# Performance work log

Hardware: AMD Instinct MI355X
Metric: run time of the kernel (lower is better)

The kernel has to match this reference:

```python
import jax, jax.numpy as jnp
import numpy as np

SEQ_LEN = 8192
VOCAB = 128000
EMB = 10   # embedding_size hard-coded in RNNLM.__init__
HID = 10   # hidden_size hard-coded


def setup_inputs() -> dict:
    key = jax.random.key(0)
    k1, k2, k3, k4, k5, k6 = jax.random.split(key, 6)
    input_batch = jax.random.randint(k1, (SEQ_LEN, 1), 0, VOCAB, dtype=jnp.int32)
    embedding = jax.random.normal(k2, (VOCAB, EMB), dtype=jnp.float32)
    # nn.Linear(input+hidden -> hidden) and nn.Linear(input+hidden -> vocab)
    W_i2h = jax.random.normal(k3, (HID, EMB + HID), dtype=jnp.float32) * 0.1
    b_i2h = jax.random.normal(k4, (HID,), dtype=jnp.float32) * 0.1
    W_i2o = jax.random.normal(k5, (VOCAB, EMB + HID), dtype=jnp.float32) * 0.1
    b_i2o = jax.random.normal(k6, (VOCAB,), dtype=jnp.float32) * 0.1
    return {
        "input_batch": input_batch,
        "embedding": embedding,
        "W_i2h": W_i2h,
        "b_i2h": b_i2h,
        "W_i2o": W_i2o,
        "b_i2o": b_i2o,
    }


def reference(input_batch, embedding, W_i2h, b_i2h, W_i2o, b_i2o):
    # Elman RNN unrolled over time via lax.scan; batch is 1 (required by the
    # original torch.cat of [B,10] embedding with [1,10] hidden state).
    def step(hidden, word_ix):
        w = embedding[word_ix]                              # (1, EMB)
        combined = jnp.concatenate([w, hidden], axis=1)     # (1, EMB+HID)
        new_hidden = combined @ W_i2h.T + b_i2h             # (1, HID)
        logits = combined @ W_i2o.T + b_i2o                 # (1, VOCAB)
        logp = jax.nn.log_softmax(logits, axis=1)
        pred = jnp.argmax(logp, axis=1).astype(jnp.float32)  # topk(1) index
        return new_hidden, pred

    hidden0 = jnp.zeros((1, HID), dtype=jnp.float32)
    _, preds = jax.lax.scan(step, hidden0, input_batch)     # preds: (SEQ_LEN, 1)
    return preds
```

## Files before the change

### kernel.cpp

```cpp
#include <hip/hip_runtime.h>

#define SEQ   8192
#define VOCAB 128000
#define L     64
#define NCH   128

#define OFF_CMB    0
#define OFF_CVEC   163840
#define OFF_AMAX   245760
#define OFF_AMAX1  262144
#define OFF_CNORM  270336
#define OFF_WPART  278528
#define OFF_WMAX   279040
#define OFF_C32    279104
#define OFF_W32    410176

#define CSL    160
#define CVSPAN 800
#define CNIT   25
#define SSL    64
#define SVSPAN 512
#define SNIT   16
#define CCAP   2048

typedef __attribute__((ext_vector_type(8))) short bf16x8;
typedef __attribute__((ext_vector_type(4))) float f32x4;

static __device__ inline unsigned short f2bf(float x) {
    unsigned u = __float_as_uint(x);
    u += 0x7FFF + ((u >> 16) & 1);
    return (unsigned short)(u >> 16);
}
static __device__ inline unsigned sortable(float x) {
    unsigned u = __float_as_uint(x);
    return (u & 0x80000000u) ? ~u : (u | 0x80000000u);
}
static __device__ inline float unsortable(unsigned k) {
    unsigned u = (k & 0x80000000u) ? (k & 0x7FFFFFFFu) : ~k;
    return __uint_as_float(u);
}

__global__ void k_prep(const int* __restrict__ ix, const float* __restrict__ emb,
                       const float* __restrict__ Wih, const float* __restrict__ bih,
                       const float* __restrict__ Wio, const float* __restrict__ bio,
                       float* __restrict__ ws) {
    int b = blockIdx.x;
    int tid = threadIdx.x;
    if (b < 32) {
        int t = b * 256 + tid;
        ((unsigned long long*)(ws + OFF_AMAX))[t] = 0ULL;
        ((unsigned*)(ws + OFF_AMAX1))[t] = 0u;

        int id = ix[t];
        float w[10];
        const float2* ep = (const float2*)(emb + (long long)id * 10);
#pragma unroll
        for (int j = 0; j < 5; j++) ((float2*)w)[j] = ep[j];
#pragma unroll
        for (int j = 0; j < 10; j++) ws[OFF_CMB + j * SEQ + t] = w[j];

        int m = t >> 6, k = t & 63;
        float* cv = ws + OFF_CVEC + (k * NCH + m) * 10;
#pragma unroll
        for (int i = 0; i < 10; i++) {
            float s = bih[i];
#pragma unroll
            for (int j = 0; j < 10; j++) s += Wih[i * 20 + j] * w[j];
            cv[i] = s;
        }
    } else {
        __shared__ float red[4];
        int bs = b - 32;
        int v = bs * 256 + tid;
        float w[20];
        const float4* r = (const float4*)(Wio + (long long)v * 20);
#pragma unroll
        for (int q = 0; q < 5; q++) ((float4*)w)[q] = r[q];
        float bv = bio[v];
        float n2 = bv * bv;
#pragma unroll
        for (int k = 0; k < 20; k++) n2 += w[k] * w[k];
        float nrm = sqrtf(n2);
        for (int off = 1; off < 64; off <<= 1)
            nrm = fmaxf(nrm, __shfl_xor(nrm, off));
        if ((tid & 63) == 0) red[tid >> 6] = nrm;
        __syncthreads();
        if (tid == 0)
            ws[OFF_WPART + bs] = fmaxf(fmaxf(red[0], red[1]), fmaxf(red[2], red[3]));

        unsigned short h[32];
#pragma unroll
        for (int k = 0; k < 20; k++) h[k] = f2bf(w[k]);
        h[20] = f2bf(bv);
#pragma unroll
        for (int k = 21; k < 32; k++) h[k] = 0;
        uint4* dst = (uint4*)((unsigned short*)(ws + OFF_W32));
#pragma unroll
        for (int i = 0; i < 4; i++) {
            uint4 u;
            u.x = (unsigned)h[8*i+0] | ((unsigned)h[8*i+1] << 16);
            u.y = (unsigned)h[8*i+2] | ((unsigned)h[8*i+3] << 16);
            u.z = (unsigned)h[8*i+4] | ((unsigned)h[8*i+5] << 16);
            u.w = (unsigned)h[8*i+6] | ((unsigned)h[8*i+7] << 16);
            dst[v * 4 + i] = u;
        }
    }
}

__global__ void k_scan(const float* __restrict__ Wih, float* __restrict__ ws) {
    __shared__ float P[100], Q[100];
    __shared__ float Dl[NCH][10];
    __shared__ float Hst[NCH][10];
    __shared__ float Hl[10];
    int tid = threadIdx.x;

    float Ar[10][10];
#pragma unroll
    for (int i = 0; i < 10; i++)
#pragma unroll
        for (int j = 0; j < 10; j++) Ar[i][j] = Wih[i * 20 + 10 + j];

    {
        int m = tid;
        float h[10];
#pragma unroll
        for (int i = 0; i < 10; i++) h[i] = 0.f;
        const float* cvb = ws + OFF_CVEC;
        float2 buf[5];
        {
            const float2* cp = (const float2*)(cvb + m * 10);
#pragma unroll
            for (int j = 0; j < 5; j++) buf[j] = cp[j];
        }
        for (int k = 0; k < L; k++) {
            float cc[10];
#pragma unroll
            for (int j = 0; j < 5; j++) { cc[2*j] = buf[j].x; cc[2*j+1] = buf[j].y; }
            if (k + 1 < L) {
                const float2* cp = (const float2*)(cvb + ((k + 1) * NCH + m) * 10);
#pragma unroll
                for (int j = 0; j < 5; j++) buf[j] = cp[j];
            }
            float nh[10];
#pragma unroll
            for (int i = 0; i < 10; i++) {
                float s = cc[i];
#pragma unroll
                for (int j = 0; j < 10; j++) s += Ar[i][j] * h[j];
                nh[i] = s;
            }
#pragma unroll
            for (int i = 0; i < 10; i++) h[i] = nh[i];
        }
#pragma unroll
        for (int i = 0; i < 10; i++) Dl[m][i] = h[i];
    }

    if (tid < 100) P[tid] = Wih[(tid / 10) * 20 + 10 + (tid % 10)];
    __syncthreads();
    for (int it = 0; it < 6; it++) {
        if (tid < 100) {
            int i = tid / 10, j = tid % 10;
            float s = 0.f;
#pragma unroll
            for (int k = 0; k < 10; k++) s += P[i * 10 + k] * P[k * 10 + j];
            Q[tid] = s;
        }
        __syncthreads();
        if (tid < 100) P[tid] = Q[tid];
        __syncthreads();
    }

    if (tid < 10) Hl[tid] = 0.f;
    __syncthreads();
    if (tid < 10) {
        int i = tid;
        float a64[10];
#pragma unroll
        for (int j = 0; j < 10; j++) a64[j] = P[i * 10 + j];
        float hc = 0.f;
        for (int m = 0; m < NCH; m++) {
            Hst[m][i] = hc;
            float s = Dl[m][i];
#pragma unroll
            for (int j = 0; j < 10; j++) s += a64[j] * Hl[j];
            Hl[i] = s;
            hc = s;
        }
    }
    __syncthreads();

    {
        int m = tid;
        float h[10];
#pragma unroll
        for (int i = 0; i < 10; i++) h[i] = Hst[m][i];
        const float* cvb = ws + OFF_CVEC;
        float2 buf[5];
        {
            const float2* cp = (const float2*)(cvb + m * 10);
#pragma unroll
            for (int j = 0; j < 5; j++) buf[j] = cp[j];
        }
        for (int k = 0; k < L; k++) {
            int tg = m * 64 + k;
            float cc[10];
#pragma unroll
            for (int j = 0; j < 5; j++) { cc[2*j] = buf[j].x; cc[2*j+1] = buf[j].y; }
            if (k + 1 < L) {
                const float2* cp = (const float2*)(cvb + ((k + 1) * NCH + m) * 10);
#pragma unroll
                for (int j = 0; j < 5; j++) buf[j] = cp[j];
            }
#pragma unroll
            for (int i = 0; i < 10; i++) ws[OFF_CMB + (10 + i) * SEQ + tg] = h[i];
            float nh[10];
#pragma unroll
            for (int i = 0; i < 10; i++) {
                float s = cc[i];
#pragma unroll
                for (int j = 0; j < 10; j++) s += Ar[i][j] * h[j];
                nh[i] = s;
            }
#pragma unroll
            for (int i = 0; i < 10; i++) h[i] = nh[i];
        }
    }
}

__global__ void k_pack_c(float* __restrict__ ws) {
    int b = blockIdx.x;
    int tid = threadIdx.x;
    if (b == 32) {
        __shared__ float red[4];
        float m = 0.f;
        for (int i = tid; i < 500; i += 256) m = fmaxf(m, ws[OFF_WPART + i]);
        for (int off = 1; off < 64; off <<= 1)
            m = fmaxf(m, __shfl_xor(m, off));
        if ((tid & 63) == 0) red[tid >> 6] = m;
        __syncthreads();
        if (tid == 0)
            ws[OFF_WMAX] = fmaxf(fmaxf(red[0], red[1]), fmaxf(red[2], red[3]));
        return;
    }
    int t = b * 256 + tid;
    float c[20];
#pragma unroll
    for (int k = 0; k < 20; k++) c[k] = ws[OFF_CMB + k * SEQ + t];
    float n2 = 1.0f;
#pragma unroll
    for (int k = 0; k < 20; k++) n2 += c[k] * c[k];
    ws[OFF_CNORM + t] = sqrtf(n2);

    unsigned short h[32];
#pragma unroll
    for (int k = 0; k < 20; k++) h[k] = f2bf(c[k]);
    h[20] = f2bf(1.0f);
#pragma unroll
    for (int k = 21; k < 32; k++) h[k] = 0;
    uint4* dst = (uint4*)((unsigned short*)(ws + OFF_C32));
#pragma unroll
    for (int i = 0; i < 4; i++) {
        uint4 u;
        u.x = (unsigned)h[8*i+0] | ((unsigned)h[8*i+1] << 16);
        u.y = (unsigned)h[8*i+2] | ((unsigned)h[8*i+3] << 16);
        u.z = (unsigned)h[8*i+4] | ((unsigned)h[8*i+5] << 16);
        u.w = (unsigned)h[8*i+6] | ((unsigned)h[8*i+7] << 16);
        dst[t * 4 + i] = u;
    }
}

__global__ __launch_bounds__(256, 4)
void k_seed(const float* __restrict__ ws, unsigned* __restrict__ amax1) {
    int tid = threadIdx.x;
    int lane = tid & 63, wid = tid >> 6, quad = lane >> 4, col = lane & 15;
    int r  = blockIdx.x & 7;
    int u  = blockIdx.x >> 3;
    int sl = r * 8 + (u & 7);
    int tb = u >> 3;
    int t0w = tb * 512 + wid * 128;
    int v0s = sl * SVSPAN;

    const unsigned short* c32 = (const unsigned short*)(ws + OFF_C32);
    const unsigned short* Wg  = (const unsigned short*)(ws + OFF_W32);

    bf16x8 a[8];
#pragma unroll
    for (int tt = 0; tt < 8; tt++)
        a[tt] = *(const bf16x8*)(c32 + (t0w + tt * 16 + col) * 32 + quad * 8);

    const f32x4 zero = {0.f, 0.f, 0.f, 0.f};
    float run[8][4];
#pragma unroll
    for (int tt = 0; tt < 8; tt++)
#pragma unroll
        for (int g = 0; g < 4; g++) run[tt][g] = -3.4e38f;

    const unsigned short* Wb = Wg + (unsigned)(v0s + col) * 32 + quad * 8;
    bf16x8 nb0 = *(const bf16x8*)(Wb);
    bf16x8 nb1 = *(const bf16x8*)(Wb + 512);

    for (int p = 0; p < SNIT; ++p) {
        bf16x8 b0 = nb0, b1 = nb1;
        int pn = (p + 1 < SNIT) ? p + 1 : p;
        const unsigned short* Wn = Wb + pn * 1024;
        nb0 = *(const bf16x8*)(Wn);
        nb1 = *(const bf16x8*)(Wn + 512);
#pragma unroll
        for (int tt = 0; tt < 8; tt++) {
            f32x4 d0 = __builtin_amdgcn_mfma_f32_16x16x32_bf16(a[tt], b0, zero, 0, 0, 0);
            f32x4 d1 = __builtin_amdgcn_mfma_f32_16x16x32_bf16(a[tt], b1, zero, 0, 0, 0);
#pragma unroll
            for (int g = 0; g < 4; g++)
                run[tt][g] = fmaxf(run[tt][g], fmaxf(d0[g], d1[g]));
        }
    }

#pragma unroll
    for (int tt = 0; tt < 8; tt++)
#pragma unroll
        for (int g = 0; g < 4; g++) {
            float r2 = run[tt][g];
            for (int off = 1; off < 16; off <<= 1)
                r2 = fmaxf(r2, __shfl_xor(r2, off));
            if (col == 0)
                atomicMax(&amax1[t0w + tt * 16 + quad * 4 + g], sortable(r2));
        }
}

__global__ __launch_bounds__(256, 4)
void k_cand(const float* __restrict__ ws, const float* __restrict__ Wio,
            const float* __restrict__ bio, const unsigned* __restrict__ amax1,
            unsigned long long* __restrict__ amax) {
    __shared__ unsigned cand[CCAP];
    __shared__ unsigned cnt;

    int tid = threadIdx.x;
    int lane = tid & 63, wid = tid >> 6, quad = lane >> 4, col = lane & 15;
    int r  = blockIdx.x & 7;
    int u  = blockIdx.x >> 3;
    int sl = r * 20 + (u % 20);
    int tb = u / 20;
    int t0w = tb * 512 + wid * 128;
    int v0s = sl * CVSPAN;
    if (tid == 0) cnt = 0;
    __syncthreads();

    const unsigned short* c32 = (const unsigned short*)(ws + OFF_C32);
    const unsigned short* Wg  = (const unsigned short*)(ws + OFF_W32);
    float wmax = ws[OFF_WMAX];

    bf16x8 a[8];
    f32x4 thrC[8];
#pragma unroll
    for (int tt = 0; tt < 8; tt++) {
        a[tt] = *(const bf16x8*)(c32 + (t0w + tt * 16 + col) * 32 + quad * 8);
#pragma unroll
        for (int g = 0; g < 4; g++) {
            int t = t0w + tt * 16 + quad * 4 + g;
            thrC[tt][g] = (0.04f * ws[OFF_CNORM + t] * wmax + 1e-5f)
                          - unsortable(amax1[t]);
        }
    }

    const unsigned short* Wb = Wg + (unsigned)(v0s + col) * 32 + quad * 8;
    bf16x8 nb0 = *(const bf16x8*)(Wb);
    bf16x8 nb1 = *(const bf16x8*)(Wb + 512);

    unsigned mask[8];
#pragma unroll
    for (int tt = 0; tt < 8; tt++) mask[tt] = 0u;

    for (int p = 0; p < CNIT; ++p) {
        bf16x8 b0 = nb0, b1 = nb1;
        int pn = (p + 1 < CNIT) ? p + 1 : p;
        const unsigned short* Wn = Wb + pn * 1024;
        nb0 = *(const bf16x8*)(Wn);
        nb1 = *(const bf16x8*)(Wn + 512);
        unsigned bit = 1u << p;
#pragma unroll
        for (int tt = 0; tt < 8; tt++) {
            f32x4 d0 = __builtin_amdgcn_mfma_f32_16x16x32_bf16(a[tt], b0, thrC[tt], 0, 0, 0);
            f32x4 d1 = __builtin_amdgcn_mfma_f32_16x16x32_bf16(a[tt], b1, thrC[tt], 0, 0, 0);
            float m1 = fmaxf(fmaxf(d0[0], d0[1]), d0[2]);
            float m2 = fmaxf(fmaxf(d0[3], d1[0]), d1[1]);
            float m3 = fmaxf(fmaxf(d1[2], d1[3]), m1);
            mask[tt] |= (fmaxf(m2, m3) >= 0.f) ? bit : 0u;
        }
    }

#pragma unroll
    for (int tt = 0; tt < 8; tt++) {
        unsigned m = mask[tt];
        for (int off = 1; off < 64; off <<= 1)
            m |= __shfl_xor(m, off);
        while (m) {
            int p = __ffs(m) - 1;
            m &= m - 1;
            const unsigned short* Wp = Wb + p * 1024;
            bf16x8 b0 = *(const bf16x8*)(Wp);
            bf16x8 b1 = *(const bf16x8*)(Wp + 512);
            f32x4 d0 = __builtin_amdgcn_mfma_f32_16x16x32_bf16(a[tt], b0, thrC[tt], 0, 0, 0);
            f32x4 d1 = __builtin_amdgcn_mfma_f32_16x16x32_bf16(a[tt], b1, thrC[tt], 0, 0, 0);
            int v0 = v0s + p * 32 + col;
#pragma unroll
            for (int g = 0; g < 4; g++) {
                unsigned t = (unsigned)(t0w + tt * 16 + quad * 4 + g);
                if (d0[g] >= 0.f) {
                    unsigned idx = atomicAdd(&cnt, 1u);
                    if (idx < CCAP) cand[idx] = (t << 17) | (unsigned)v0;
                }
                if (d1[g] >= 0.f) {
                    unsigned idx = atomicAdd(&cnt, 1u);
                    if (idx < CCAP) cand[idx] = (t << 17) | (unsigned)(v0 + 16);
                }
            }
        }
    }

    __syncthreads();
    unsigned n = cnt < CCAP ? cnt : CCAP;
    const float* cmb = ws + OFF_CMB;
    for (unsigned i = tid; i < n; i += 256) {
        unsigned e = cand[i];
        int t = (int)(e >> 17);
        int v = (int)(e & 0x1FFFFu);
        const float* wr = Wio + (long long)v * 20;
        float ex = bio[v];
#pragma unroll
        for (int k = 0; k < 20; k++)
            ex = fmaf(wr[k], cmb[k * SEQ + t], ex);
        unsigned key = sortable(ex);
        unsigned long long packed =
            ((unsigned long long)key << 32) | (unsigned)(VOCAB - v);
        unsigned long long cur = amax[t];
        if (packed > cur)
            atomicMax(&amax[t], packed);
    }
}

__global__ void k_out(const unsigned long long* __restrict__ amax,
                      float* __restrict__ out) {
    int t = blockIdx.x * blockDim.x + threadIdx.x;
    if (t >= SEQ) return;
    unsigned long long p = amax[t];
    int idx = VOCAB - (int)(p & 0xFFFFFFFFu);
    out[t] = (float)idx;
}

extern "C" void kernel_launch(void* const* d_in, const int* in_sizes, int n_in,
                              void* d_out, int out_size, void* d_ws, size_t ws_size,
                              hipStream_t stream) {
    (void)in_sizes; (void)n_in; (void)out_size; (void)ws_size;
    const int*   ix  = (const int*)d_in[0];
    const float* emb = (const float*)d_in[1];
    const float* Wih = (const float*)d_in[2];
    const float* bih = (const float*)d_in[3];
    const float* Wio = (const float*)d_in[4];
    const float* bio = (const float*)d_in[5];
    float* out = (float*)d_out;
    float* ws  = (float*)d_ws;
    unsigned long long* amax = (unsigned long long*)(ws + OFF_AMAX);
    unsigned* amax1 = (unsigned*)(ws + OFF_AMAX1);

    hipLaunchKernelGGL(k_prep,   dim3(532),      dim3(256), 0, stream, ix, emb, Wih, bih, Wio, bio, ws);
    hipLaunchKernelGGL(k_scan,   dim3(1),        dim3(128), 0, stream, Wih, ws);
    hipLaunchKernelGGL(k_pack_c, dim3(33),       dim3(256), 0, stream, ws);
    hipLaunchKernelGGL(k_seed,   dim3(16 * SSL), dim3(256), 0, stream, ws, amax1);
    hipLaunchKernelGGL(k_cand,   dim3(8 * 320),  dim3(256), 0, stream, ws, Wio, bio, amax1, amax);
    hipLaunchKernelGGL(k_out,    dim3(SEQ / 256),dim3(256), 0, stream, amax, out);
}
```

Before: 302.4 us.

## Fold per-row threshold into MFMA operand via extra K column

A new small kernel writes each timestep's pruning threshold, rounded to bf16, into a spare K slot of the packed combined-vector matrix. The weight rows get -1 in the matching slot, so the MFMA now produces logit minus threshold directly and can use a zero accumulator. This drops the per-thread threshold loads and the eight per-tile accumulator registers, and replaces the eight per-tile masks with a single mask. The rescan now reruns all eight tiles for any hit chunk, which costs extra MFMAs, and it adds one more kernel launch. The directed rounding (the increment applied to negative values) is meant to keep the bf16 threshold conservative, but the threshold now carries bf16 precision.

Result: no change. 306.5 us (+1.4%).

```diff
diff --git a/kernel.cpp b/kernel.cpp
--- a/kernel.cpp
+++ b/kernel.cpp
@@ -92,8 +92,9 @@
 #pragma unroll
         for (int k = 0; k < 20; k++) h[k] = f2bf(w[k]);
         h[20] = f2bf(bv);
-#pragma unroll
-        for (int k = 21; k < 32; k++) h[k] = 0;
+        h[21] = 0xBF80;
+#pragma unroll
+        for (int k = 22; k < 32; k++) h[k] = 0;
         uint4* dst = (uint4*)((unsigned short*)(ws + OFF_W32));
 #pragma unroll
         for (int i = 0; i < 4; i++) {
@@ -328,9 +329,19 @@
         }
 }
 
+__global__ void k_thr(float* __restrict__ ws, const unsigned* __restrict__ amax1) {
+    int t = blockIdx.x * 256 + threadIdx.x;
+    float wmax = ws[OFF_WMAX];
+    float thr = unsortable(amax1[t]) - (0.04f * ws[OFF_CNORM + t] * wmax + 1e-5f);
+    unsigned u = __float_as_uint(thr);
+    unsigned short h = (unsigned short)(u >> 16);
+    if ((u & 0xFFFFu) && (u & 0x80000000u)) h++;
+    ((unsigned short*)(ws + OFF_C32))[t * 32 + 21] = h;
+}
+
 __global__ __launch_bounds__(256, 4)
 void k_cand(const float* __restrict__ ws, const float* __restrict__ Wio,
-            const float* __restrict__ bio, const unsigned* __restrict__ amax1,
+            const float* __restrict__ bio,
             unsigned long long* __restrict__ amax) {
     __shared__ unsigned cand[CCAP];
     __shared__ unsigned cnt;
@@ -348,28 +359,18 @@
 
     const unsigned short* c32 = (const unsigned short*)(ws + OFF_C32);
     const unsigned short* Wg  = (const unsigned short*)(ws + OFF_W32);
-    float wmax = ws[OFF_WMAX];
 
     bf16x8 a[8];
-    f32x4 thrC[8];
-#pragma unroll
-    for (int tt = 0; tt < 8; tt++) {
+#pragma unroll
+    for (int tt = 0; tt < 8; tt++)
         a[tt] = *(const bf16x8*)(c32 + (t0w + tt * 16 + col) * 32 + quad * 8);
-#pragma unroll
-        for (int g = 0; g < 4; g++) {
-            int t = t0w + tt * 16 + quad * 4 + g;
-            thrC[tt][g] = (0.04f * ws[OFF_CNORM + t] * wmax + 1e-5f)
-                          - unsortable(amax1[t]);
-        }
-    }
-
+
+    const f32x4 zero = {0.f, 0.f, 0.f, 0.f};
     const unsigned short* Wb = Wg + (unsigned)(v0s + col) * 32 + quad * 8;
     bf16x8 nb0 = *(const bf16x8*)(Wb);
     bf16x8 nb1 = *(const bf16x8*)(Wb + 512);
 
-    unsigned mask[8];
-#pragma unroll
-    for (int tt = 0; tt < 8; tt++) mask[tt] = 0u;
+    unsigned mask = 0u;
 
     for (int p = 0; p < CNIT; ++p) {
         bf16x8 b0 = nb0, b1 = nb1;
@@ -377,21 +378,21 @@
         const unsigned short* Wn = Wb + pn * 1024;
         nb0 = *(const bf16x8*)(Wn);
         nb1 = *(const bf16x8*)(Wn + 512);
-        unsigned bit = 1u << p;
+        float gm = -3.4e38f;
 #pragma unroll
         for (int tt = 0; tt < 8; tt++) {
-            f32x4 d0 = __builtin_amdgcn_mfma_f32_16x16x32_bf16(a[tt], b0, thrC[tt], 0, 0, 0);
-            f32x4 d1 = __builtin_amdgcn_mfma_f32_16x16x32_bf16(a[tt], b1, thrC[tt], 0, 0, 0);
+            f32x4 d0 = __builtin_amdgcn_mfma_f32_16x16x32_bf16(a[tt], b0, zero, 0, 0, 0);
+            f32x4 d1 = __builtin_amdgcn_mfma_f32_16x16x32_bf16(a[tt], b1, zero, 0, 0, 0);
             float m1 = fmaxf(fmaxf(d0[0], d0[1]), d0[2]);
             float m2 = fmaxf(fmaxf(d0[3], d1[0]), d1[1]);
             float m3 = fmaxf(fmaxf(d1[2], d1[3]), m1);
-            mask[tt] |= (fmaxf(m2, m3) >= 0.f) ? bit : 0u;
-        }
-    }
-
-#pragma unroll
-    for (int tt = 0; tt < 8; tt++) {
-        unsigned m = mask[tt];
+            gm = fmaxf(gm, fmaxf(m2, m3));
+        }
+        mask |= (gm >= 0.f) ? (1u << p) : 0u;
+    }
+
+    {
+        unsigned m = mask;
         for (int off = 1; off < 64; off <<= 1)
             m |= __shfl_xor(m, off);
         while (m) {
@@ -400,19 +401,22 @@
             const unsigned short* Wp = Wb + p * 1024;
             bf16x8 b0 = *(const bf16x8*)(Wp);
             bf16x8 b1 = *(const bf16x8*)(Wp + 512);
-            f32x4 d0 = __builtin_amdgcn_mfma_f32_16x16x32_bf16(a[tt], b0, thrC[tt], 0, 0, 0);
-            f32x4 d1 = __builtin_amdgcn_mfma_f32_16x16x32_bf16(a[tt], b1, thrC[tt], 0, 0, 0);
             int v0 = v0s + p * 32 + col;
 #pragma unroll
-            for (int g = 0; g < 4; g++) {
-                unsigned t = (unsigned)(t0w + tt * 16 + quad * 4 + g);
-                if (d0[g] >= 0.f) {
-                    unsigned idx = atomicAdd(&cnt, 1u);
-                    if (idx < CCAP) cand[idx] = (t << 17) | (unsigned)v0;
-                }
-                if (d1[g] >= 0.f) {
-                    unsigned idx = atomicAdd(&cnt, 1u);
-                    if (idx < CCAP) cand[idx] = (t << 17) | (unsigned)(v0 + 16);
+            for (int tt = 0; tt < 8; tt++) {
+                f32x4 d0 = __builtin_amdgcn_mfma_f32_16x16x32_bf16(a[tt], b0, zero, 0, 0, 0);
+                f32x4 d1 = __builtin_amdgcn_mfma_f32_16x16x32_bf16(a[tt], b1, zero, 0, 0, 0);
+#pragma unroll
+                for (int g = 0; g < 4; g++) {
+                    unsigned t = (unsigned)(t0w + tt * 16 + quad * 4 + g);
+                    if (d0[g] >= 0.f) {
+                        unsigned idx = atomicAdd(&cnt, 1u);
+                        if (idx < CCAP) cand[idx] = (t << 17) | (unsigned)v0;
+                    }
+                    if (d1[g] >= 0.f) {
+                        unsigned idx = atomicAdd(&cnt, 1u);
+                        if (idx < CCAP) cand[idx] = (t << 17) | (unsigned)(v0 + 16);
+                    }
                 }
             }
         }
@@ -467,6 +471,7 @@
     hipLaunchKernelGGL(k_scan,   dim3(1),        dim3(128), 0, stream, Wih, ws);
     hipLaunchKernelGGL(k_pack_c, dim3(33),       dim3(256), 0, stream, ws);
     hipLaunchKernelGGL(k_seed,   dim3(16 * SSL), dim3(256), 0, stream, ws, amax1);
-    hipLaunchKernelGGL(k_cand,   dim3(8 * 320),  dim3(256), 0, stream, ws, Wio, bio, amax1, amax);
+    hipLaunchKernelGGL(k_thr,    dim3(32),       dim3(256), 0, stream, ws, amax1);
+    hipLaunchKernelGGL(k_cand,   dim3(8 * 320),  dim3(256), 0, stream, ws, Wio, bio, amax);
     hipLaunchKernelGGL(k_out,    dim3(SEQ / 256),dim3(256), 0, stream, amax, out);
 }
```

## Fuse C packing into seed kernel and fold threshold into MFMA operand

Applied to the files above, without the earlier changes.

Removes the k_pack_c launch. Each seed block now packs its own 512-row slice of combined vectors to bf16 before its MFMA pass, and each cand block recomputes the global weight-norm max itself. The per-row threshold is folded into the GEMM by storing it as bf16 in an unused K slot of the A operand, with a -1 in the matching W slot, so the accumulator input becomes zero and the thrC registers go away. Occupancy for k_cand is raised to 8 blocks per SM. The risks are redundant packing writes, since 64 blocks write the same slice, bf16 rounding of the threshold (rounded upward for negatives), and any cross-block ordering issue in the fused pack.

Result: slower. 364.4 us (+20.5%).

```diff
diff --git a/kernel.cpp b/kernel.cpp
--- a/kernel.cpp
+++ b/kernel.cpp
@@ -92,8 +92,9 @@
 #pragma unroll
         for (int k = 0; k < 20; k++) h[k] = f2bf(w[k]);
         h[20] = f2bf(bv);
-#pragma unroll
-        for (int k = 21; k < 32; k++) h[k] = 0;
+        h[21] = 0xBF80;
+#pragma unroll
+        for (int k = 22; k < 32; k++) h[k] = 0;
         uint4* dst = (uint4*)((unsigned short*)(ws + OFF_W32));
 #pragma unroll
         for (int i = 0; i < 4; i++) {
@@ -228,50 +229,8 @@
     }
 }
 
-__global__ void k_pack_c(float* __restrict__ ws) {
-    int b = blockIdx.x;
-    int tid = threadIdx.x;
-    if (b == 32) {
-        __shared__ float red[4];
-        float m = 0.f;
-        for (int i = tid; i < 500; i += 256) m = fmaxf(m, ws[OFF_WPART + i]);
-        for (int off = 1; off < 64; off <<= 1)
-            m = fmaxf(m, __shfl_xor(m, off));
-        if ((tid & 63) == 0) red[tid >> 6] = m;
-        __syncthreads();
-        if (tid == 0)
-            ws[OFF_WMAX] = fmaxf(fmaxf(red[0], red[1]), fmaxf(red[2], red[3]));
-        return;
-    }
-    int t = b * 256 + tid;
-    float c[20];
-#pragma unroll
-    for (int k = 0; k < 20; k++) c[k] = ws[OFF_CMB + k * SEQ + t];
-    float n2 = 1.0f;
-#pragma unroll
-    for (int k = 0; k < 20; k++) n2 += c[k] * c[k];
-    ws[OFF_CNORM + t] = sqrtf(n2);
-
-    unsigned short h[32];
-#pragma unroll
-    for (int k = 0; k < 20; k++) h[k] = f2bf(c[k]);
-    h[20] = f2bf(1.0f);
-#pragma unroll
-    for (int k = 21; k < 32; k++) h[k] = 0;
-    uint4* dst = (uint4*)((unsigned short*)(ws + OFF_C32));
-#pragma unroll
-    for (int i = 0; i < 4; i++) {
-        uint4 u;
-        u.x = (unsigned)h[8*i+0] | ((unsigned)h[8*i+1] << 16);
-        u.y = (unsigned)h[8*i+2] | ((unsigned)h[8*i+3] << 16);
-        u.z = (unsigned)h[8*i+4] | ((unsigned)h[8*i+5] << 16);
-        u.w = (unsigned)h[8*i+6] | ((unsigned)h[8*i+7] << 16);
-        dst[t * 4 + i] = u;
-    }
-}
-
 __global__ __launch_bounds__(256, 4)
-void k_seed(const float* __restrict__ ws, unsigned* __restrict__ amax1) {
+void k_seedpack(float* __restrict__ ws, unsigned* __restrict__ amax1) {
     int tid = threadIdx.x;
     int lane = tid & 63, wid = tid >> 6, quad = lane >> 4, col = lane & 15;
     int r  = blockIdx.x & 7;
@@ -281,6 +240,38 @@
     int t0w = tb * 512 + wid * 128;
     int v0s = sl * SVSPAN;
 
+    {
+        int tbase = tb * 512;
+        uint4* dst = (uint4*)((unsigned short*)(ws + OFF_C32));
+        for (int i = tid; i < 512; i += 256) {
+            int t = tbase + i;
+            float c[20];
+#pragma unroll
+            for (int k = 0; k < 20; k++) c[k] = ws[OFF_CMB + k * SEQ + t];
+            float n2 = 1.0f;
+#pragma unroll
+            for (int k = 0; k < 20; k++) n2 += c[k] * c[k];
+            ws[OFF_CNORM + t] = sqrtf(n2);
+
+            unsigned short h[32];
+#pragma unroll
+            for (int k = 0; k < 20; k++) h[k] = f2bf(c[k]);
+            h[20] = f2bf(1.0f);
+#pragma unroll
+            for (int k = 21; k < 32; k++) h[k] = 0;
+#pragma unroll
+            for (int q = 0; q < 4; q++) {
+                uint4 v;
+                v.x = (unsigned)h[8*q+0] | ((unsigned)h[8*q+1] << 16);
+                v.y = (unsigned)h[8*q+2] | ((unsigned)h[8*q+3] << 16);
+                v.z = (unsigned)h[8*q+4] | ((unsigned)h[8*q+5] << 16);
+                v.w = (unsigned)h[8*q+6] | ((unsigned)h[8*q+7] << 16);
+                dst[t * 4 + q] = v;
+            }
+        }
+    }
+    __syncthreads();
+
     const unsigned short* c32 = (const unsigned short*)(ws + OFF_C32);
     const unsigned short* Wg  = (const unsigned short*)(ws + OFF_W32);
 
@@ -328,12 +319,14 @@
         }
 }
 
-__global__ __launch_bounds__(256, 4)
+__global__ __launch_bounds__(256, 8)
 void k_cand(const float* __restrict__ ws, const float* __restrict__ Wio,
             const float* __restrict__ bio, const unsigned* __restrict__ amax1,
             unsigned long long* __restrict__ amax) {
     __shared__ unsigned cand[CCAP];
     __shared__ unsigned cnt;
+    __shared__ float red4[4];
+    __shared__ float swmax;
 
     int tid = threadIdx.x;
     int lane = tid & 63, wid = tid >> 6, quad = lane >> 4, col = lane & 15;
@@ -344,25 +337,39 @@
     int t0w = tb * 512 + wid * 128;
     int v0s = sl * CVSPAN;
     if (tid == 0) cnt = 0;
-    __syncthreads();
+
+    {
+        float m = 0.f;
+        for (int i = tid; i < 500; i += 256) m = fmaxf(m, ws[OFF_WPART + i]);
+        for (int off = 1; off < 64; off <<= 1)
+            m = fmaxf(m, __shfl_xor(m, off));
+        if ((tid & 63) == 0) red4[tid >> 6] = m;
+        __syncthreads();
+        if (tid == 0)
+            swmax = fmaxf(fmaxf(red4[0], red4[1]), fmaxf(red4[2], red4[3]));
+        __syncthreads();
+    }
+    float wmax = swmax;
 
     const unsigned short* c32 = (const unsigned short*)(ws + OFF_C32);
     const unsigned short* Wg  = (const unsigned short*)(ws + OFF_W32);
-    float wmax = ws[OFF_WMAX];
 
     bf16x8 a[8];
-    f32x4 thrC[8];
 #pragma unroll
     for (int tt = 0; tt < 8; tt++) {
         a[tt] = *(const bf16x8*)(c32 + (t0w + tt * 16 + col) * 32 + quad * 8);
-#pragma unroll
-        for (int g = 0; g < 4; g++) {
-            int t = t0w + tt * 16 + quad * 4 + g;
-            thrC[tt][g] = (0.04f * ws[OFF_CNORM + t] * wmax + 1e-5f)
-                          - unsortable(amax1[t]);
-        }
-    }
-
+        if (quad == 2) {
+            int t = t0w + tt * 16 + col;
+            float thr = unsortable(amax1[t]) -
+                        (0.04f * ws[OFF_CNORM + t] * wmax + 1e-5f);
+            unsigned uu = __float_as_uint(thr);
+            unsigned short h = (unsigned short)(uu >> 16);
+            if ((uu & 0xFFFFu) && (uu & 0x80000000u)) h++;
+            a[tt][5] = (short)h;
+        }
+    }
+
+    const f32x4 zero = {0.f, 0.f, 0.f, 0.f};
     const unsigned short* Wb = Wg + (unsigned)(v0s + col) * 32 + quad * 8;
     bf16x8 nb0 = *(const bf16x8*)(Wb);
     bf16x8 nb1 = *(const bf16x8*)(Wb + 512);
@@ -380,8 +387,8 @@
         unsigned bit = 1u << p;
 #pragma unroll
         for (int tt = 0; tt < 8; tt++) {
-            f32x4 d0 = __builtin_amdgcn_mfma_f32_16x16x32_bf16(a[tt], b0, thrC[tt], 0, 0, 0);
-            f32x4 d1 = __builtin_amdgcn_mfma_f32_16x16x32_bf16(a[tt], b1, thrC[tt], 0, 0, 0);
+            f32x4 d0 = __builtin_amdgcn_mfma_f32_16x16x32_bf16(a[tt], b0, zero, 0, 0, 0);
+            f32x4 d1 = __builtin_amdgcn_mfma_f32_16x16x32_bf16(a[tt], b1, zero, 0, 0, 0);
             float m1 = fmaxf(fmaxf(d0[0], d0[1]), d0[2]);
             float m2 = fmaxf(fmaxf(d0[3], d1[0]), d1[1]);
             float m3 = fmaxf(fmaxf(d1[2], d1[3]), m1);
@@ -400,8 +407,8 @@
             const unsigned short* Wp = Wb + p * 1024;
             bf16x8 b0 = *(const bf16x8*)(Wp);
             bf16x8 b1 = *(const bf16x8*)(Wp + 512);
-            f32x4 d0 = __builtin_amdgcn_mfma_f32_16x16x32_bf16(a[tt], b0, thrC[tt], 0, 0, 0);
-            f32x4 d1 = __builtin_amdgcn_mfma_f32_16x16x32_bf16(a[tt], b1, thrC[tt], 0, 0, 0);
+            f32x4 d0 = __builtin_amdgcn_mfma_f32_16x16x32_bf16(a[tt], b0, zero, 0, 0, 0);
+            f32x4 d1 = __builtin_amdgcn_mfma_f32_16x16x32_bf16(a[tt], b1, zero, 0, 0, 0);
             int v0 = v0s + p * 32 + col;
 #pragma unroll
             for (int g = 0; g < 4; g++) {
@@ -463,10 +470,9 @@
     unsigned long long* amax = (unsigned long long*)(ws + OFF_AMAX);
     unsigned* amax1 = (unsigned*)(ws + OFF_AMAX1);
 
-    hipLaunchKernelGGL(k_prep,   dim3(532),      dim3(256), 0, stream, ix, emb, Wih, bih, Wio, bio, ws);
-    hipLaunchKernelGGL(k_scan,   dim3(1),        dim3(128), 0, stream, Wih, ws);
-    hipLaunchKernelGGL(k_pack_c, dim3(33),       dim3(256), 0, stream, ws);
-    hipLaunchKernelGGL(k_seed,   dim3(16 * SSL), dim3(256), 0, stream, ws, amax1);
-    hipLaunchKernelGGL(k_cand,   dim3(8 * 320),  dim3(256), 0, stream, ws, Wio, bio, amax1, amax);
-    hipLaunchKernelGGL(k_out,    dim3(SEQ / 256),dim3(256), 0, stream, amax, out);
-}
+    hipLaunchKernelGGL(k_prep,     dim3(532),      dim3(256), 0, stream, ix, emb, Wih, bih, Wio, bio, ws);
+    hipLaunchKernelGGL(k_scan,     dim3(1),        dim3(128), 0, stream, Wih, ws);
+    hipLaunchKernelGGL(k_seedpack, dim3(16 * SSL), dim3(256), 0, stream, ws, amax1);
+    hipLaunchKernelGGL(k_cand,     dim3(8 * 320),  dim3(256), 0, stream, ws, Wio, bio, amax1, amax);
+    hipLaunchKernelGGL(k_out,      dim3(SEQ / 256),dim3(256), 0, stream, amax, out);
+}
```
